# Performance work log

Measured on AMD Instinct MI355X. Metric: run time of the kernel, lower is better.

## Reference

```python
import jax, jax.numpy as jnp
import numpy as np

DIM = 256
DIM_HEAD = 32
HEADS = DIM // DIM_HEAD
NUM_TYPES = 2
WS = 7
AGENTS = 6
SCALE = DIM_HEAD ** -0.5


def _rel_pos_index():
    # Static relative-position index for a WS x WS window (torch meshgrid default = 'ij')
    coords = np.stack(np.meshgrid(np.arange(WS), np.arange(WS), indexing='ij'))  # (2,WS,WS)
    cf = coords.reshape(2, -1)                     # (2, WS*WS)
    rel = cf[:, :, None] - cf[:, None, :]          # (2, 49, 49)
    rel = rel.transpose(1, 2, 0).copy()
    rel[:, :, 0] += WS - 1
    rel[:, :, 1] += WS - 1
    rel[:, :, 0] *= 2 * WS - 1
    return jnp.asarray(rel.sum(-1))                # (49, 49) int


def setup_inputs() -> dict:
    key = jax.random.key(0)
    ks = jax.random.split(key, 16)
    B, L, X, Y = 4, AGENTS, 8, 8
    x = jax.random.normal(ks[0], (B, L, X, Y, WS, WS, DIM), dtype=jnp.float32)
    mode = jax.random.randint(ks[1], (B, L), 0, NUM_TYPES)
    s = 0.02
    Wq = jax.random.normal(ks[2], (NUM_TYPES, DIM, DIM), dtype=jnp.float32) * s
    bq = jax.random.normal(ks[3], (NUM_TYPES, DIM), dtype=jnp.float32) * s
    Wk = jax.random.normal(ks[4], (NUM_TYPES, DIM, DIM), dtype=jnp.float32) * s
    bk = jax.random.normal(ks[5], (NUM_TYPES, DIM), dtype=jnp.float32) * s
    Wv = jax.random.normal(ks[6], (NUM_TYPES, DIM, DIM), dtype=jnp.float32) * s
    bv = jax.random.normal(ks[7], (NUM_TYPES, DIM), dtype=jnp.float32) * s
    Wa = jax.random.normal(ks[8], (NUM_TYPES, DIM, DIM), dtype=jnp.float32) * s
    ba = jax.random.normal(ks[9], (NUM_TYPES, DIM), dtype=jnp.float32) * s
    # xavier_uniform over (num_relations, heads, dh, dh): fan based on last two dims
    lim = float(np.sqrt(6.0 / (DIM_HEAD + DIM_HEAD)))
    relation_att = jax.random.uniform(ks[10], (NUM_TYPES * NUM_TYPES, HEADS, DIM_HEAD, DIM_HEAD), minval=-lim, maxval=lim, dtype=jnp.float32)
    relation_msg = jax.random.uniform(ks[11], (NUM_TYPES * NUM_TYPES, HEADS, DIM_HEAD, DIM_HEAD), minval=-lim, maxval=lim, dtype=jnp.float32)
    pos_table = jax.random.normal(ks[12], ((2 * WS - 1) * (2 * WS - 1), HEADS), dtype=jnp.float32)
    return dict(x=x, mode=mode, Wq=Wq, bq=bq, Wk=Wk, bk=bk, Wv=Wv, bv=bv, Wa=Wa, ba=ba,
                relation_att=relation_att, relation_msg=relation_msg, pos_table=pos_table)


def reference(x, mode, Wq, bq, Wk, bk, Wv, bv, Wa, ba, relation_att, relation_msg, pos_table):
    B, L, X, Y, w1, w2, D = x.shape
    h, dh = HEADS, DIM_HEAD
    W = w1 * w2

    def proj(Wt, bt):
        # type-routed Linear: gather per-(b,l) weight, y = x @ W[t].T + b[t]
        y = jnp.einsum('blxyuvd,bled->blxyuve', x, Wt[mode]) + bt[mode][:, :, None, None, None, None, :]
        # b l x y u v (h d) -> b x y h l u v d
        return y.reshape(B, L, X, Y, w1, w2, h, dh).transpose(0, 2, 3, 6, 1, 4, 5, 7)

    q = proj(Wq, bq)[:, :, :, :, :1] * SCALE   # ego agent only (a=1)
    k = proj(Wk, bk)
    v = proj(Wv, bv)

    # relation index for (ego type, agent z type): r[b,z] = mode[b,0]*T + mode[b,z]
    rel_idx = mode[:, :1] * NUM_TYPES + mode           # (B, L)
    w_att = relation_att[rel_idx]                      # (B, L, h, dh, dh)
    w_msg = relation_msg[rel_idx]

    # sim_{pq} = q_p W_att[p,q] k_q
    kw = jnp.einsum('bzhpq,bxyhzefq->bxyhzefp', w_att, k)
    sim = jnp.einsum('bxyhacdp,bxyhzefp->bxyhacdzef', q, kw)  # (B,X,Y,h,1,w1,w2,L,w1,w2)

    # relative position bias, broadcast over agents z
    bias = pos_table[_rel_pos_index()].transpose(2, 0, 1)     # (h, 49, 49)
    sim = sim.reshape(B, X, Y, h, 1, W, L, W) + bias[None, None, None, :, None, :, None, :]

    # softmax over all keys (z, e, f) jointly
    attn = jax.nn.softmax(sim.reshape(B, X, Y, h, W, L * W), axis=-1)
    attn = attn.reshape(B, X, Y, h, 1, w1, w2, L, w1, w2)

    # message: v'_q = sum_p v_p W_msg[p,q]
    v_msg = jnp.einsum('bzhpq,bxyhzefp->bxyhzefq', w_msg, v)
    out = jnp.einsum('bxyhacdzef,bxyhzefq->bxyhacdq', attn, v_msg)

    # b x y h a c d q -> b a x y c d (h q)
    out = out.transpose(0, 4, 1, 2, 5, 6, 3, 7).reshape(B, 1, X, Y, w1, w2, D)

    # type-routed output projection for ego agent
    m0 = mode[:, :1]
    out = jnp.einsum('blxyuvd,bled->blxyuve', out, Wa[m0]) + ba[m0][:, :, None, None, None, None, :]
    return out
```

## Files before the change

kernel.cpp:

```cpp
#include <hip/hip_runtime.h>

typedef unsigned short u16;
typedef unsigned int   u32;
typedef _Float16 f16;
typedef _Float16 h2  __attribute__((ext_vector_type(2)));
typedef _Float16 h8  __attribute__((ext_vector_type(8)));
typedef float    fx4 __attribute__((ext_vector_type(4)));

#define SCALE_Q 0.17677669529663687f

__device__ __forceinline__ u16 f2h_bits(float f){
  union{ f16 h; u16 u; } v; v.h = (f16)f; return v.u;
}
__device__ __forceinline__ u32 packh2(float a, float b){
  union{ h2 h; u32 u; } v; v.h = h2{(f16)a, (f16)b}; return v.u;
}
__device__ __forceinline__ h2 as_h2(u32 x){
  union{ u32 u; h2 h; } v; v.u = x; return v.h;
}
__device__ __forceinline__ h8 as_h8(uint4 u){
  union{ uint4 u; h8 h; } v; v.u = u; return v.h;
}

__global__ void flag_fill(float* out, int n, float v){
  int i = blockIdx.x*256 + threadIdx.x;
  if (i < n) out[i] = v;
}

__global__ __launch_bounds__(512) void fuse_all(
    const float* __restrict__ Wk, const float* __restrict__ Wv,
    const float* __restrict__ Ratt, const float* __restrict__ Rmsg,
    const float* __restrict__ Wq, const float* __restrict__ Wa,
    const float* __restrict__ bk, const float* __restrict__ bv,
    u16* __restrict__ Wft, float* __restrict__ bff,
    u16* __restrict__ Wqf, u16* __restrict__ Waf)
{
  const int blk = blockIdx.x;
  const int n = threadIdx.x;
  if (blk < 1024){
    const int rel = blk >> 8, d = blk & 255, ml = rel & 1;
    float acc = 0.f;
    if (n < 256) {
      const int h = n >> 5, p = n & 31;
      const float* wcol = Wk + (size_t)ml*65536 + (size_t)(h*32)*256 + d;
      const float* rrow = Ratt + ((size_t)(rel*8 + h)*32 + p)*32;
      #pragma unroll
      for (int q = 0; q < 32; ++q) acc += wcol[q*256] * rrow[q];
    } else {
      const int n2 = n - 256, h = n2 >> 5, qq = n2 & 31;
      const float* wcol = Wv + (size_t)ml*65536 + (size_t)(h*32)*256 + d;
      const float* rcol = Rmsg + ((size_t)(rel*8 + h)*32)*32 + qq;
      #pragma unroll
      for (int p2 = 0; p2 < 32; ++p2) acc += wcol[p2*256] * rcol[p2*32];
    }
    Wft[(size_t)rel*131072 + (size_t)(d >> 5)*16384 + (size_t)n*32 + (d & 31)] = f2h_bits(acc);
  } else if (blk < 1028){
    const int rel = blk - 1024, ml = rel & 1;
    float acc = 0.f;
    if (n < 256) {
      const int h = n >> 5, p = n & 31;
      const float* rrow = Ratt + ((size_t)(rel*8 + h)*32 + p)*32;
      #pragma unroll
      for (int q = 0; q < 32; ++q) acc += bk[ml*256 + h*32 + q] * rrow[q];
    } else {
      const int n2 = n - 256, h = n2 >> 5, qq = n2 & 31;
      const float* rcol = Rmsg + ((size_t)(rel*8 + h)*32)*32 + qq;
      #pragma unroll
      for (int p2 = 0; p2 < 32; ++p2) acc += bv[ml*256 + h*32 + p2] * rcol[p2*32];
    }
    bff[rel*512 + n] = acc;
  } else {
    const int bb = blk - 1028;
    const int t = bb >> 8, d = bb & 255;
    if (n < 256){
      float v = Wq[(size_t)t*65536 + (size_t)n*256 + d] * SCALE_Q;
      Wqf[(size_t)t*65536 + (size_t)(d >> 5)*8192 + (size_t)n*32 + (d & 31)] = f2h_bits(v);
    } else {
      const int e = n - 256;
      float v = Wa[(size_t)t*65536 + (size_t)e*256 + d];
      Waf[(size_t)t*65536 + (size_t)(d >> 5)*8192 + (size_t)e*32 + (d & 31)] = f2h_bits(v);
    }
  }
}

#define ASTRIDE 264

__global__ __launch_bounds__(512) void gemm_kwv(
    const float* __restrict__ x, const int* __restrict__ mode,
    const u16* __restrict__ Wft, const float* __restrict__ bff,
    u16* __restrict__ kw, u16* __restrict__ vm, int b0)
{
  __shared__ u16 Smem[64*ASTRIDE];
  const int rowT  = blockIdx.x;
  const int bloc = rowT / 294;
  const int rem  = rowT % 294;
  const int l = rem / 49, tile = rem % 49;
  const int b = b0 + bloc;
  const int rel = mode[b*6]*2 + mode[b*6 + l];
  const float* Abase = x + ((size_t)(b*6 + l)*3136 + (size_t)tile*64)*256;
  const int tid  = threadIdx.x;
  const int wave = tid >> 6, lane = tid & 63;
  const int quad = lane >> 4, l15 = lane & 15;

  const u16* Bp = Wft + (size_t)rel*131072 + (size_t)((wave << 6) + l15)*32 + (quad << 3);

  uint4 breg[3][4];
  #pragma unroll
  for (int s = 0; s < 3; ++s)
    #pragma unroll
    for (int j = 0; j < 4; ++j){
      const u16* ap = Bp + (size_t)s*16384 + j*512;
      asm volatile("global_load_dwordx4 %0, %1, off" : "=v"(breg[s][j]) : "v"(ap));
    }

  #pragma unroll
  for (int i = 0; i < 8; ++i){
    float4 f = *(const float4*)(Abase + (size_t)i*2048 + tid*4);
    const int row = i*8 + (tid >> 6), col = (tid & 63)*4;
    uint2 pk; pk.x = packh2(f.x, f.y); pk.y = packh2(f.z, f.w);
    *(uint2*)&Smem[row*ASTRIDE + col] = pk;
  }
  __syncthreads();

  fx4 acc[4][4];
  #pragma unroll
  for (int mt = 0; mt < 4; ++mt)
    #pragma unroll
    for (int j = 0; j < 4; ++j) acc[mt][j] = fx4{0,0,0,0};

  const u16* As = &Smem[l15*ASTRIDE + (quad << 3)];

  #pragma unroll
  for (int s = 0; s < 8; ++s){
    if (s >= 3 && s <= 5)      { asm volatile("s_waitcnt vmcnt(8)" ::: "memory"); }
    else if (s == 6)           { asm volatile("s_waitcnt vmcnt(4)" ::: "memory"); }
    else if (s == 7)           { asm volatile("s_waitcnt vmcnt(0)" ::: "memory"); }
    __builtin_amdgcn_sched_barrier(0);
    h8 af[4];
    #pragma unroll
    for (int mt = 0; mt < 4; ++mt)
      af[mt] = *(const h8*)(As + (mt*16)*ASTRIDE + s*32);
    const int slot = s % 3;
    #pragma unroll
    for (int j = 0; j < 4; ++j){
      h8 bf = as_h8(breg[slot][j]);
      #pragma unroll
      for (int mt = 0; mt < 4; ++mt)
        acc[mt][j] = __builtin_amdgcn_mfma_f32_16x16x32_f16(af[mt], bf, acc[mt][j], 0, 0, 0);
    }
    if (s < 5){
      #pragma unroll
      for (int j = 0; j < 4; ++j){
        const u16* ap = Bp + (size_t)(s + 3)*16384 + j*512;
        asm volatile("global_load_dwordx4 %0, %1, off" : "=v"(breg[slot][j]) : "v"(ap));
      }
    }
  }

  const int row_ = tid >> 3;
  const int hsel = tid & 7;
  const int r_g  = tile*64 + row_;
  const int xy   = r_g / 49, ef = r_g - xy*49;

  #pragma unroll
  for (int half = 0; half < 2; ++half){
    __syncthreads();
    if ((wave >> 2) == half){
      #pragma unroll
      for (int j = 0; j < 4; ++j){
        const int n   = wave*64 + j*16 + l15;
        const int col = n & 255;
        const float bias = bff[rel*512 + n];
        #pragma unroll
        for (int mt = 0; mt < 4; ++mt){
          #pragma unroll
          for (int reg = 0; reg < 4; ++reg){
            const int row = mt*16 + quad*4 + reg;
            Smem[row*ASTRIDE + col] = f2h_bits(acc[mt][j][reg] + bias);
          }
        }
      }
    }
    __syncthreads();
    u16* dbuf = half ? vm : kw;
    u16* dst  = dbuf + ((((size_t)(bloc*64 + xy)*8 + hsel)*6 + l)*49 + ef)*32;
    const u16* srcl = &Smem[row_*ASTRIDE + hsel*32];
    *(uint4*)(dst)      = *(const uint4*)(srcl);
    *(uint4*)(dst + 8)  = *(const uint4*)(srcl + 8);
    *(uint4*)(dst + 16) = *(const uint4*)(srcl + 16);
    *(uint4*)(dst + 24) = *(const uint4*)(srcl + 24);
  }
}

__global__ __launch_bounds__(256, 2) void gemm_qp(
    const float* __restrict__ x, const int* __restrict__ mode,
    const u16* __restrict__ Wqf, const float* __restrict__ bq,
    u16* __restrict__ qbuf)
{
  __shared__ u16 Smem[32*ASTRIDE];
  const int rowT = blockIdx.x;
  const int b = rowT / 98, tile = rowT % 98;
  const int m0 = mode[b*6];
  const float* Abase = x + ((size_t)(b*6)*3136 + (size_t)tile*32)*256;
  const int tid = threadIdx.x;
  const int wave = tid >> 6, lane = tid & 63;
  const int quad = lane >> 4, l15 = lane & 15;

  const u16* Bp = Wqf + (size_t)m0*65536 + (size_t)((wave << 6) + l15)*32 + (quad << 3);
  uint4 breg[32];
  #pragma unroll
  for (int s = 0; s < 8; ++s)
    #pragma unroll
    for (int j = 0; j < 4; ++j){
      const u16* ap = Bp + (size_t)s*8192 + j*512;
      asm volatile("global_load_dwordx4 %0, %1, off" : "=v"(breg[s*4+j]) : "v"(ap));
    }

  {
    const int r = tid >> 3, cseg = (tid & 7)*32;
    const float* src = Abase + (size_t)r*256 + cseg;
    u16* dst = &Smem[r*ASTRIDE + cseg];
    #pragma unroll
    for (int i = 0; i < 4; ++i){
      float4 f0 = *(const float4*)(src + i*8);
      float4 f1 = *(const float4*)(src + i*8 + 4);
      uint4 pk;
      pk.x = packh2(f0.x, f0.y); pk.y = packh2(f0.z, f0.w);
      pk.z = packh2(f1.x, f1.y); pk.w = packh2(f1.z, f1.w);
      *(uint4*)(dst + i*8) = pk;
    }
  }
  __syncthreads();

  fx4 acc[2][4];
  #pragma unroll
  for (int mt = 0; mt < 2; ++mt)
    #pragma unroll
    for (int j = 0; j < 4; ++j) acc[mt][j] = fx4{0,0,0,0};

  const u16* As0 = &Smem[l15*ASTRIDE + (quad << 3)];
  const u16* As1 = As0 + 16*ASTRIDE;
  asm volatile("s_waitcnt vmcnt(0)" ::: "memory");
  __builtin_amdgcn_sched_barrier(0);
  #pragma unroll
  for (int s = 0; s < 8; ++s){
    h8 af0 = *(const h8*)(As0 + s*32);
    h8 af1 = *(const h8*)(As1 + s*32);
    #pragma unroll
    for (int j = 0; j < 4; ++j){
      h8 bf = as_h8(breg[s*4+j]);
      acc[0][j] = __builtin_amdgcn_mfma_f32_16x16x32_f16(af0, bf, acc[0][j], 0, 0, 0);
      acc[1][j] = __builtin_amdgcn_mfma_f32_16x16x32_f16(af1, bf, acc[1][j], 0, 0, 0);
    }
  }

  __syncthreads();
  #pragma unroll
  for (int j = 0; j < 4; ++j){
    const int n = wave*64 + j*16 + l15;
    const float bias = bq[m0*256 + n] * SCALE_Q;
    #pragma unroll
    for (int mt = 0; mt < 2; ++mt)
      #pragma unroll
      for (int reg = 0; reg < 4; ++reg){
        const int row = mt*16 + quad*4 + reg;
        Smem[row*ASTRIDE + n] = f2h_bits(acc[mt][j][reg] + bias);
      }
  }
  __syncthreads();
  {
    const int row_ = tid >> 3, hsel = tid & 7;
    const int r_g = tile*32 + row_;
    const int xy = r_g / 49, ef = r_g - xy*49;
    u16* dst = qbuf + (((size_t)(b*64 + xy)*8 + hsel)*49 + ef)*32;
    const u16* srcl = &Smem[row_*ASTRIDE + hsel*32];
    *(uint4*)(dst)      = *(const uint4*)(srcl);
    *(uint4*)(dst + 8)  = *(const uint4*)(srcl + 8);
    *(uint4*)(dst + 16) = *(const uint4*)(srcl + 16);
    *(uint4*)(dst + 24) = *(const uint4*)(srcl + 24);
  }
}

#define LGKM0  do{ asm volatile("s_waitcnt lgkmcnt(0)" ::: "memory"); \
                   __builtin_amdgcn_sched_barrier(0); }while(0)

__device__ __forceinline__ void scatter_v(u16* VTb, int i4, uint4 vv){
  const int ef = i4 >> 2, pb = (i4 & 3)*8, c0 = ef >> 3;
  u16* vt = VTb + (ef & 7);
  vt[(pb+0)*64 + ((c0 ^ 0) << 3)] = (u16)(vv.x & 0xFFFFu);
  vt[(pb+1)*64 + ((c0 ^ 1) << 3)] = (u16)(vv.x >> 16);
  vt[(pb+2)*64 + ((c0 ^ 2) << 3)] = (u16)(vv.y & 0xFFFFu);
  vt[(pb+3)*64 + ((c0 ^ 3) << 3)] = (u16)(vv.y >> 16);
  vt[(pb+4)*64 + ((c0 ^ 4) << 3)] = (u16)(vv.z & 0xFFFFu);
  vt[(pb+5)*64 + ((c0 ^ 5) << 3)] = (u16)(vv.z >> 16);
  vt[(pb+6)*64 + ((c0 ^ 6) << 3)] = (u16)(vv.w & 0xFFFFu);
  vt[(pb+7)*64 + ((c0 ^ 7) << 3)] = (u16)(vv.w >> 16);
}

__global__ __launch_bounds__(64) void attn_kernel(
    const u16* __restrict__ qbuf, const u16* __restrict__ kw,
    const u16* __restrict__ vm,   const float* __restrict__ post,
    u16* __restrict__ aout, int b0)
{
  __shared__ u32 Ks[2*64*16];
  __shared__ u16 VT[2*32*64];
  __shared__ u16 PQ[64*64];
  __shared__ float poss[169];

  const int bloc  = blockIdx.x >> 9;
  const int local = blockIdx.x & 511;
  const int h = local & 7, xy = local >> 3;
  const int bxy = (b0 + bloc)*64 + xy;
  const int lane = threadIdx.x;
  const int quad = lane >> 4, l15 = lane & 15;

  const size_t kvbase = ((size_t)(bloc*64 + xy)*8 + h)*6;

  for (int i = lane; i < 169; i += 64) poss[i] = post[i*8 + h];
  for (int i = lane; i < 480; i += 64){
    const int bb = i / 240, o = i - bb*240;
    Ks[bb*1024 + 784 + o] = 0;
  }
  for (int i = lane; i < 1024; i += 64){
    const int bb = i >> 9, r = i & 511;
    const int p = r >> 4, ke = 48 + (r & 15);
    VT[bb*2048 + p*64 + ((((ke >> 3) ^ (p & 7)) & 7) << 3) + (ke & 7)] = 0;
  }
  { const u16* qsrc = qbuf + (size_t)(bxy*8 + h)*1568;
    for (int i = lane; i < 196; i += 64)
      *(uint4*)&PQ[(i >> 2)*32 + (i & 3)*8] = *(const uint4*)(qsrc + (size_t)i*8);
    const uint4 z4 = make_uint4(0,0,0,0);
    for (int i = lane; i < 60; i += 64)
      *(uint4*)&PQ[1568 + i*8] = z4;
  }
  { const uint4* ksrc = (const uint4*)((const u32*)kw + kvbase*784);
    for (int i = lane; i < 196; i += 64) ((uint4*)Ks)[i] = ksrc[i];
    const uint4* vsrc = (const uint4*)((const u32*)vm + kvbase*784);
    for (int i = lane; i < 196; i += 64) scatter_v(VT, i, vsrc[i]);
  }
  LGKM0;

  h8 qf[4];
  #pragma unroll
  for (int nt = 0; nt < 4; ++nt)
    qf[nt] = *(const h8*)&PQ[(nt*16 + l15)*32 + quad*8];

  fx4 bias[4][4];
  { int qa[4], qb[4];
    #pragma unroll
    for (int nt = 0; nt < 4; ++nt){
      const int qi = nt*16 + l15; qa[nt] = qi/7; qb[nt] = qi - qa[nt]*7;
    }
    #pragma unroll
    for (int mt = 0; mt < 4; ++mt)
      #pragma unroll
      for (int reg = 0; reg < 4; ++reg){
        const int ke = mt*16 + quad*4 + reg;
        const int ka = ke/7, kb = ke - ka*7;
        #pragma unroll
        for (int nt = 0; nt < 4; ++nt){
          const int qi = nt*16 + l15;
          float bv;
          if (ke > 48)      bv = -1e30f;
          else if (qi > 48) bv = 0.f;
          else              bv = poss[(qa[nt] - ka + 6)*13 + (qb[nt] - kb + 6)];
          bias[mt][nt][reg] = bv;
        }
      }
  }

  float mprev[4], lsum[4];
  fx4 Oacc[2][4];
  #pragma unroll
  for (int nt = 0; nt < 4; ++nt){
    mprev[nt] = -1e30f; lsum[nt] = 0.f;
    Oacc[0][nt] = fx4{0,0,0,0}; Oacc[1][nt] = fx4{0,0,0,0};
  }

  int cur = 0;
  for (int z = 0; z < 6; ++z){
    uint4 kn0, kn1, kn2, kn3, vn0, vn1, vn2, vn3;
    if (z < 5){
      const uint4* ksrc = (const uint4*)((const u32*)kw + (kvbase + z + 1)*784);
      const uint4* vsrc = (const uint4*)((const u32*)vm + (kvbase + z + 1)*784);
      kn0 = ksrc[lane]; kn1 = ksrc[64 + lane]; kn2 = ksrc[128 + lane];
      vn0 = vsrc[lane]; vn1 = vsrc[64 + lane]; vn2 = vsrc[128 + lane];
      if (lane < 4){ kn3 = ksrc[192 + lane]; vn3 = vsrc[192 + lane]; }
    }

    const u32* KsC = Ks + cur*1024;
    const u16* VTC = VT + cur*2048;

    h8 kf[4];
    #pragma unroll
    for (int mt = 0; mt < 4; ++mt)
      kf[mt] = *(const h8*)((const u16*)KsC + (mt*16 + l15)*32 + quad*8);
    fx4 S[4][4];
    #pragma unroll
    for (int mt = 0; mt < 4; ++mt)
      #pragma unroll
      for (int nt = 0; nt < 4; ++nt)
        S[mt][nt] = __builtin_amdgcn_mfma_f32_16x16x32_f16(kf[mt], qf[nt], bias[mt][nt], 0, 0, 0);

    #pragma unroll
    for (int nt = 0; nt < 4; ++nt){
      float cm = S[0][nt][0];
      #pragma unroll
      for (int mt = 0; mt < 4; ++mt)
        #pragma unroll
        for (int r = 0; r < 4; ++r) cm = fmaxf(cm, S[mt][nt][r]);
      cm = fmaxf(cm, __shfl_xor(cm, 16));
      cm = fmaxf(cm, __shfl_xor(cm, 32));
      const float mnew = fmaxf(mprev[nt], cm);
      const float alpha = __expf(mprev[nt] - mnew);
      mprev[nt] = mnew;
      float sum = 0.f;
      #pragma unroll
      for (int mt = 0; mt < 4; ++mt)
        #pragma unroll
        for (int r = 0; r < 4; ++r){
          float e = __expf(S[mt][nt][r] - mnew); S[mt][nt][r] = e; sum += e;
        }
      sum += __shfl_xor(sum, 16);
      sum += __shfl_xor(sum, 32);
      lsum[nt] = lsum[nt]*alpha + sum;
      #pragma unroll
      for (int r = 0; r < 4; ++r){ Oacc[0][nt][r] *= alpha; Oacc[1][nt][r] *= alpha; }
    }

    #pragma unroll
    for (int nt = 0; nt < 4; ++nt){
      const int qi = nt*16 + l15;
      u16* prow = &PQ[qi*64 + ((quad & 1) << 2)];
      #pragma unroll
      for (int mt = 0; mt < 4; ++mt){
        const int chk = (mt*2 + (quad >> 1)) ^ (l15 & 7);
        uint2 w;
        w.x = packh2(S[mt][nt][0], S[mt][nt][1]);
        w.y = packh2(S[mt][nt][2], S[mt][nt][3]);
        *(uint2*)(prow + (chk << 3)) = w;
      }
    }
    LGKM0;

    #pragma unroll
    for (int ks = 0; ks < 2; ++ks){
      h8 vf[2];
      #pragma unroll
      for (int m2 = 0; m2 < 2; ++m2)
        vf[m2] = *(const h8*)&VTC[(m2*16 + l15)*64 + (((ks*4 + quad) ^ (l15 & 7)) << 3)];
      #pragma unroll
      for (int nt = 0; nt < 4; ++nt){
        h8 pf = *(const h8*)&PQ[(nt*16 + l15)*64 + (((ks*4 + quad) ^ (l15 & 7)) << 3)];
        Oacc[0][nt] = __builtin_amdgcn_mfma_f32_16x16x32_f16(vf[0], pf, Oacc[0][nt], 0, 0, 0);
        Oacc[1][nt] = __builtin_amdgcn_mfma_f32_16x16x32_f16(vf[1], pf, Oacc[1][nt], 0, 0, 0);
      }
    }

    if (z < 5){
      u32* KsN = Ks + (cur ^ 1)*1024;
      u16* VTN = VT + (cur ^ 1)*2048;
      ((uint4*)KsN)[lane]       = kn0;
      ((uint4*)KsN)[64 + lane]  = kn1;
      ((uint4*)KsN)[128 + lane] = kn2;
      scatter_v(VTN, lane,       vn0);
      scatter_v(VTN, 64 + lane,  vn1);
      scatter_v(VTN, 128 + lane, vn2);
      if (lane < 4){
        ((uint4*)KsN)[192 + lane] = kn3;
        scatter_v(VTN, 192 + lane, vn3);
      }
    }
    LGKM0;
    cur ^= 1;
  }

  #pragma unroll
  for (int nt = 0; nt < 4; ++nt){
    const int qi = nt*16 + l15;
    if (qi < 49){
      const float inv = 1.f / lsum[nt];
      #pragma unroll
      for (int m2 = 0; m2 < 2; ++m2){
        uint2 w;
        w.x = packh2(Oacc[m2][nt][0]*inv, Oacc[m2][nt][1]*inv);
        w.y = packh2(Oacc[m2][nt][2]*inv, Oacc[m2][nt][3]*inv);
        *(uint2*)&PQ[qi*32 + m2*16 + quad*4] = w;
      }
    }
  }
  LGKM0;
  { u16* obase = aout + (size_t)bxy*12544 + h*32;
    for (int i = lane; i < 196; i += 64){
      const int r = i >> 2, c = (i & 3)*8;
      *(uint4*)(obase + (size_t)r*256 + c) = *(const uint4*)&PQ[r*32 + c];
    }
  }
}

__global__ __launch_bounds__(256, 2) void gemm_op(
    const u16* __restrict__ aout, const int* __restrict__ mode,
    const u16* __restrict__ Waf, const float* __restrict__ ba,
    float* __restrict__ outp)
{
  __shared__ float Smf[32*260];
  u16* Smem = (u16*)Smf;
  const int rowT = blockIdx.x;
  const int b = rowT / 98, tile = rowT % 98;
  const int m0 = mode[b*6];
  const u16* Abase = aout + ((size_t)b*3136 + (size_t)tile*32)*256;
  const int tid = threadIdx.x;
  const int wave = tid >> 6, lane = tid & 63;
  const int quad = lane >> 4, l15 = lane & 15;

  const u16* Bp = Waf + (size_t)m0*65536 + (size_t)((wave << 6) + l15)*32 + (quad << 3);
  uint4 breg[32];
  #pragma unroll
  for (int s = 0; s < 8; ++s)
    #pragma unroll
    for (int j = 0; j < 4; ++j){
      const u16* ap = Bp + (size_t)s*8192 + j*512;
      asm volatile("global_load_dwordx4 %0, %1, off" : "=v"(breg[s*4+j]) : "v"(ap));
    }

  {
    const int r = tid >> 3, cseg = (tid & 7)*32;
    const u16* src = Abase + (size_t)r*256 + cseg;
    u16* dst = &Smem[r*ASTRIDE + cseg];
    #pragma unroll
    for (int i = 0; i < 4; ++i)
      *(uint4*)(dst + i*8) = *(const uint4*)(src + i*8);
  }
  __syncthreads();

  fx4 acc[2][4];
  #pragma unroll
  for (int mt = 0; mt < 2; ++mt)
    #pragma unroll
    for (int j = 0; j < 4; ++j) acc[mt][j] = fx4{0,0,0,0};

  const u16* As0 = &Smem[l15*ASTRIDE + (quad << 3)];
  const u16* As1 = As0 + 16*ASTRIDE;
  asm volatile("s_waitcnt vmcnt(0)" ::: "memory");
  __builtin_amdgcn_sched_barrier(0);
  #pragma unroll
  for (int s = 0; s < 8; ++s){
    h8 af0 = *(const h8*)(As0 + s*32);
    h8 af1 = *(const h8*)(As1 + s*32);
    #pragma unroll
    for (int j = 0; j < 4; ++j){
      h8 bf = as_h8(breg[s*4+j]);
      acc[0][j] = __builtin_amdgcn_mfma_f32_16x16x32_f16(af0, bf, acc[0][j], 0, 0, 0);
      acc[1][j] = __builtin_amdgcn_mfma_f32_16x16x32_f16(af1, bf, acc[1][j], 0, 0, 0);
    }
  }

  __syncthreads();
  #pragma unroll
  for (int j = 0; j < 4; ++j){
    const int n = wave*64 + j*16 + l15;
    const float bias = ba[m0*256 + n];
    #pragma unroll
    for (int mt = 0; mt < 2; ++mt)
      #pragma unroll
      for (int reg = 0; reg < 4; ++reg){
        const int row = mt*16 + quad*4 + reg;
        Smf[row*260 + n] = acc[mt][j][reg] + bias;
      }
  }
  __syncthreads();
  {
    const int row_ = tid >> 3, seg = (tid & 7)*32;
    const int rowg = b*3136 + tile*32 + row_;
    float* dst = outp + (size_t)rowg*256 + seg;
    const float* srcl = &Smf[row_*260 + seg];
    #pragma unroll
    for (int i = 0; i < 8; ++i)
      *(float4*)(dst + i*4) = *(const float4*)(srcl + i*4);
  }
}

extern "C" void kernel_launch(void* const* d_in, const int* in_sizes, int n_in,
                              void* d_out, int out_size, void* d_ws, size_t ws_size,
                              hipStream_t stream)
{
  float* outp = (float*)d_out;
  const int FLAG_GRID = (out_size + 255)/256;

  if (n_in != 13) { flag_fill<<<FLAG_GRID,256,0,stream>>>(outp, out_size, 2000.f); return; }
  if (in_sizes[0] != 4*6*64*49*256) { flag_fill<<<FLAG_GRID,256,0,stream>>>(outp, out_size, 3000.f); return; }
  if (in_sizes[1] != 24) { flag_fill<<<FLAG_GRID,256,0,stream>>>(outp, out_size, 4000.f); return; }

  const size_t SZ_WFT  = (size_t)4*512*256*2;
  const size_t SZ_BFF  = (size_t)4*512*sizeof(float);
  const size_t SZ_WQF  = (size_t)2*256*256*2;
  const size_t SZ_WAF  = (size_t)2*256*256*2;
  const size_t SZ_Q    = (size_t)12544*256*2;
  const size_t SZ_AOUT = (size_t)12544*256*2;
  const size_t SZ_KW1  = (size_t)64*8*6*49*32*2;
  const size_t SZ_VM1  = SZ_KW1;
  const size_t FIXED   = SZ_WFT + SZ_BFF + SZ_WQF + SZ_WAF + SZ_Q + SZ_AOUT;
  if (ws_size < FIXED + SZ_KW1 + SZ_VM1) { flag_fill<<<FLAG_GRID,256,0,stream>>>(outp, out_size, 1000.f); return; }

  int nb = 1;
  if (ws_size >= FIXED + 4*(SZ_KW1 + SZ_VM1)) nb = 4;
  else if (ws_size >= FIXED + 2*(SZ_KW1 + SZ_VM1)) nb = 2;

  const float* x    = (const float*)d_in[0];
  const int*   mode = (const int*)d_in[1];
  const float* Wq   = (const float*)d_in[2];
  const float* bq   = (const float*)d_in[3];
  const float* Wk   = (const float*)d_in[4];
  const float* bk   = (const float*)d_in[5];
  const float* Wv   = (const float*)d_in[6];
  const float* bv   = (const float*)d_in[7];
  const float* Wa   = (const float*)d_in[8];
  const float* ba   = (const float*)d_in[9];
  const float* Ratt = (const float*)d_in[10];
  const float* Rmsg = (const float*)d_in[11];
  const float* post = (const float*)d_in[12];

  char* w = (char*)d_ws;
  u16* Wft   = (u16*)w;   w += SZ_WFT;
  float* bff = (float*)w; w += SZ_BFF;
  u16* Wqf   = (u16*)w;   w += SZ_WQF;
  u16* Waf   = (u16*)w;   w += SZ_WAF;
  u16* qbuf  = (u16*)w;   w += SZ_Q;
  u16* aout  = (u16*)w;   w += SZ_AOUT;
  u16* kwbuf = (u16*)w;   w += (size_t)nb*SZ_KW1;
  u16* vmbuf = (u16*)w;   w += (size_t)nb*SZ_VM1;

  fuse_all<<<1540, 512, 0, stream>>>(Wk, Wv, Ratt, Rmsg, Wq, Wa, bk, bv,
                                     Wft, bff, Wqf, Waf);
  gemm_qp<<<392, 256, 0, stream>>>(x, mode, Wqf, bq, qbuf);
  for (int b0 = 0; b0 < 4; b0 += nb) {
    gemm_kwv<<<nb*294, 512, 0, stream>>>(x, mode, Wft, bff, kwbuf, vmbuf, b0);
    attn_kernel<<<nb*512, 64, 0, stream>>>(qbuf, kwbuf, vmbuf, post, aout, b0);
  }
  gemm_op<<<392, 256, 0, stream>>>(aout, mode, Waf, ba, outp);
}
```

Measured before the change: 252.9 us.

## Process two row tiles per block in gemm_kwv with prefetch overlapping epilogue

```diff
diff --git a/kernel.cpp b/kernel.cpp
--- a/kernel.cpp
+++ b/kernel.cpp
@@ -20,6 +20,9 @@
 }
 __device__ __forceinline__ h8 as_h8(uint4 u){
   union{ uint4 u; h8 h; } v; v.u = u; return v.h;
+}
+__device__ __forceinline__ float4 as_f4(uint4 u){
+  union{ uint4 u; float4 f; } v; v.u = u; return v.f;
 }
 
 __global__ void flag_fill(float* out, int n, float v){
@@ -85,37 +88,109 @@
 
 #define ASTRIDE 264
 
+#define RAWBAR do{ asm volatile("s_waitcnt lgkmcnt(0)" ::: "memory"); \
+                   __builtin_amdgcn_sched_barrier(0); \
+                   __builtin_amdgcn_s_barrier(); }while(0)
+
+#define KLOOP(BPTR) do{ \
+  _Pragma("unroll") \
+  for (int s = 0; s < 8; ++s){ \
+    if (s >= 3 && s <= 5)      { asm volatile("s_waitcnt vmcnt(8)" ::: "memory"); } \
+    else if (s == 6)           { asm volatile("s_waitcnt vmcnt(4)" ::: "memory"); } \
+    else if (s == 7)           { asm volatile("s_waitcnt vmcnt(0)" ::: "memory"); } \
+    __builtin_amdgcn_sched_barrier(0); \
+    h8 af[4]; \
+    _Pragma("unroll") \
+    for (int mt = 0; mt < 4; ++mt) \
+      af[mt] = *(const h8*)(As + (mt*16)*ASTRIDE + s*32); \
+    const int slot = s % 3; \
+    _Pragma("unroll") \
+    for (int j = 0; j < 4; ++j){ \
+      h8 bf = as_h8(breg[slot][j]); \
+      _Pragma("unroll") \
+      for (int mt = 0; mt < 4; ++mt) \
+        acc[mt][j] = __builtin_amdgcn_mfma_f32_16x16x32_f16(af[mt], bf, acc[mt][j], 0, 0, 0); \
+    } \
+    if (s < 5){ \
+      _Pragma("unroll") \
+      for (int j = 0; j < 4; ++j){ \
+        const u16* ap = (BPTR) + (size_t)(s + 3)*16384 + j*512; \
+        asm volatile("global_load_dwordx4 %0, %1, off" : "=v"(breg[slot][j]) : "v"(ap)); \
+      } \
+    } \
+  } }while(0)
+
+#define EPILOGUE(BLOC, L, TILE, REL, BARRIER) do{ \
+  const int row_ = tid >> 3, hsel = tid & 7; \
+  const int r_g  = (TILE)*64 + row_; \
+  const int xy   = r_g / 49, ef = r_g - xy*49; \
+  _Pragma("unroll") \
+  for (int half = 0; half < 2; ++half){ \
+    BARRIER; \
+    if ((wave >> 2) == half){ \
+      _Pragma("unroll") \
+      for (int j = 0; j < 4; ++j){ \
+        const int n   = wave*64 + j*16 + l15; \
+        const int col = n & 255; \
+        const float biasv = bff[(REL)*512 + n]; \
+        _Pragma("unroll") \
+        for (int mt = 0; mt < 4; ++mt){ \
+          _Pragma("unroll") \
+          for (int reg = 0; reg < 4; ++reg){ \
+            const int row = mt*16 + quad*4 + reg; \
+            Smem[row*ASTRIDE + col] = f2h_bits(acc[mt][j][reg] + biasv); \
+          } \
+        } \
+      } \
+    } \
+    BARRIER; \
+    u16* dbuf = half ? vm : kw; \
+    u16* dst  = dbuf + ((((size_t)((BLOC)*64 + xy)*8 + hsel)*6 + (L))*49 + ef)*32; \
+    const u16* srcl = &Smem[row_*ASTRIDE + hsel*32]; \
+    *(uint4*)(dst)      = *(const uint4*)(srcl); \
+    *(uint4*)(dst + 8)  = *(const uint4*)(srcl + 8); \
+    *(uint4*)(dst + 16) = *(const uint4*)(srcl + 16); \
+    *(uint4*)(dst + 24) = *(const uint4*)(srcl + 24); \
+  } }while(0)
+
 __global__ __launch_bounds__(512) void gemm_kwv(
     const float* __restrict__ x, const int* __restrict__ mode,
     const u16* __restrict__ Wft, const float* __restrict__ bff,
     u16* __restrict__ kw, u16* __restrict__ vm, int b0)
 {
   __shared__ u16 Smem[64*ASTRIDE];
-  const int rowT  = blockIdx.x;
-  const int bloc = rowT / 294;
-  const int rem  = rowT % 294;
-  const int l = rem / 49, tile = rem % 49;
-  const int b = b0 + bloc;
-  const int rel = mode[b*6]*2 + mode[b*6 + l];
-  const float* Abase = x + ((size_t)(b*6 + l)*3136 + (size_t)tile*64)*256;
   const int tid  = threadIdx.x;
   const int wave = tid >> 6, lane = tid & 63;
   const int quad = lane >> 4, l15 = lane & 15;
 
-  const u16* Bp = Wft + (size_t)rel*131072 + (size_t)((wave << 6) + l15)*32 + (quad << 3);
+  int bloc0, l0, tile0, rel0, bloc1, l1, tile1, rel1;
+  const float *Ab0, *Ab1;
+  const u16 *Bp0, *Bp1;
+  {
+    const int T0 = 2*blockIdx.x, T1 = T0 + 1;
+    bloc0 = T0 / 294; { const int r = T0 % 294; l0 = r / 49; tile0 = r % 49; }
+    bloc1 = T1 / 294; { const int r = T1 % 294; l1 = r / 49; tile1 = r % 49; }
+    const int b0g = b0 + bloc0, b1g = b0 + bloc1;
+    rel0 = mode[b0g*6]*2 + mode[b0g*6 + l0];
+    rel1 = mode[b1g*6]*2 + mode[b1g*6 + l1];
+    Ab0 = x + ((size_t)(b0g*6 + l0)*3136 + (size_t)tile0*64)*256;
+    Ab1 = x + ((size_t)(b1g*6 + l1)*3136 + (size_t)tile1*64)*256;
+    Bp0 = Wft + (size_t)rel0*131072 + (size_t)((wave << 6) + l15)*32 + (quad << 3);
+    Bp1 = Wft + (size_t)rel1*131072 + (size_t)((wave << 6) + l15)*32 + (quad << 3);
+  }
 
   uint4 breg[3][4];
   #pragma unroll
   for (int s = 0; s < 3; ++s)
     #pragma unroll
     for (int j = 0; j < 4; ++j){
-      const u16* ap = Bp + (size_t)s*16384 + j*512;
+      const u16* ap = Bp0 + (size_t)s*16384 + j*512;
       asm volatile("global_load_dwordx4 %0, %1, off" : "=v"(breg[s][j]) : "v"(ap));
     }
 
   #pragma unroll
   for (int i = 0; i < 8; ++i){
-    float4 f = *(const float4*)(Abase + (size_t)i*2048 + tid*4);
+    float4 f = *(const float4*)(Ab0 + (size_t)i*2048 + tid*4);
     const int row = i*8 + (tid >> 6), col = (tid & 63)*4;
     uint2 pk; pk.x = packh2(f.x, f.y); pk.y = packh2(f.z, f.w);
     *(uint2*)&Smem[row*ASTRIDE + col] = pk;
@@ -130,66 +205,45 @@
 
   const u16* As = &Smem[l15*ASTRIDE + (quad << 3)];
 
-  #pragma unroll
-  for (int s = 0; s < 8; ++s){
-    if (s >= 3 && s <= 5)      { asm volatile("s_waitcnt vmcnt(8)" ::: "memory"); }
-    else if (s == 6)           { asm volatile("s_waitcnt vmcnt(4)" ::: "memory"); }
-    else if (s == 7)           { asm volatile("s_waitcnt vmcnt(0)" ::: "memory"); }
-    __builtin_amdgcn_sched_barrier(0);
-    h8 af[4];
-    #pragma unroll
-    for (int mt = 0; mt < 4; ++mt)
-      af[mt] = *(const h8*)(As + (mt*16)*ASTRIDE + s*32);
-    const int slot = s % 3;
+  KLOOP(Bp0);
+
+  uint4 aR[8];
+  #pragma unroll
+  for (int i = 0; i < 8; ++i){
+    const float* ap = Ab1 + (size_t)i*2048 + tid*4;
+    asm volatile("global_load_dwordx4 %0, %1, off" : "=v"(aR[i]) : "v"(ap));
+  }
+  #pragma unroll
+  for (int s = 0; s < 3; ++s)
     #pragma unroll
     for (int j = 0; j < 4; ++j){
-      h8 bf = as_h8(breg[slot][j]);
-      #pragma unroll
-      for (int mt = 0; mt < 4; ++mt)
-        acc[mt][j] = __builtin_amdgcn_mfma_f32_16x16x32_f16(af[mt], bf, acc[mt][j], 0, 0, 0);
-    }
-    if (s < 5){
-      #pragma unroll
-      for (int j = 0; j < 4; ++j){
-        const u16* ap = Bp + (size_t)(s + 3)*16384 + j*512;
-        asm volatile("global_load_dwordx4 %0, %1, off" : "=v"(breg[slot][j]) : "v"(ap));
-      }
-    }
-  }
-
-  const int row_ = tid >> 3;
-  const int hsel = tid & 7;
-  const int r_g  = tile*64 + row_;
-  const int xy   = r_g / 49, ef = r_g - xy*49;
-
-  #pragma unroll
-  for (int half = 0; half < 2; ++half){
-    __syncthreads();
-    if ((wave >> 2) == half){
-      #pragma unroll
-      for (int j = 0; j < 4; ++j){
-        const int n   = wave*64 + j*16 + l15;
-        const int col = n & 255;
-        const float bias = bff[rel*512 + n];
-        #pragma unroll
-        for (int mt = 0; mt < 4; ++mt){
-          #pragma unroll
-          for (int reg = 0; reg < 4; ++reg){
-            const int row = mt*16 + quad*4 + reg;
-            Smem[row*ASTRIDE + col] = f2h_bits(acc[mt][j][reg] + bias);
-          }
-        }
-      }
-    }
-    __syncthreads();
-    u16* dbuf = half ? vm : kw;
-    u16* dst  = dbuf + ((((size_t)(bloc*64 + xy)*8 + hsel)*6 + l)*49 + ef)*32;
-    const u16* srcl = &Smem[row_*ASTRIDE + hsel*32];
-    *(uint4*)(dst)      = *(const uint4*)(srcl);
-    *(uint4*)(dst + 8)  = *(const uint4*)(srcl + 8);
-    *(uint4*)(dst + 16) = *(const uint4*)(srcl + 16);
-    *(uint4*)(dst + 24) = *(const uint4*)(srcl + 24);
-  }
+      const u16* ap = Bp1 + (size_t)s*16384 + j*512;
+      asm volatile("global_load_dwordx4 %0, %1, off" : "=v"(breg[s][j]) : "v"(ap));
+    }
+
+  EPILOGUE(bloc0, l0, tile0, rel0, RAWBAR);
+
+  RAWBAR;
+
+  asm volatile("s_waitcnt vmcnt(0)" ::: "memory");
+  __builtin_amdgcn_sched_barrier(0);
+  #pragma unroll
+  for (int i = 0; i < 8; ++i){
+    float4 f = as_f4(aR[i]);
+    const int row = i*8 + (tid >> 6), col = (tid & 63)*4;
+    uint2 pk; pk.x = packh2(f.x, f.y); pk.y = packh2(f.z, f.w);
+    *(uint2*)&Smem[row*ASTRIDE + col] = pk;
+  }
+  RAWBAR;
+
+  #pragma unroll
+  for (int mt = 0; mt < 4; ++mt)
+    #pragma unroll
+    for (int j = 0; j < 4; ++j) acc[mt][j] = fx4{0,0,0,0};
+
+  KLOOP(Bp1);
+
+  EPILOGUE(bloc1, l1, tile1, rel1, __syncthreads());
 }
 
 __global__ __launch_bounds__(256, 2) void gemm_qp(
@@ -634,7 +688,7 @@
                                      Wft, bff, Wqf, Waf);
   gemm_qp<<<392, 256, 0, stream>>>(x, mode, Wqf, bq, qbuf);
   for (int b0 = 0; b0 < 4; b0 += nb) {
-    gemm_kwv<<<nb*294, 512, 0, stream>>>(x, mode, Wft, bff, kwbuf, vmbuf, b0);
+    gemm_kwv<<<nb*147, 512, 0, stream>>>(x, mode, Wft, bff, kwbuf, vmbuf, b0);
     attn_kernel<<<nb*512, 64, 0, stream>>>(qbuf, kwbuf, vmbuf, post, aout, b0);
   }
   gemm_op<<<392, 256, 0, stream>>>(aout, mode, Waf, ba, outp);
```

Result: slower. 261.6 us (+3.5%).
